# Performance work log

Hardware: AMD Instinct MI355X
Metric: run time of the kernel (lower is better)

The kernel has to match this reference:

```python
import jax, jax.numpy as jnp
import numpy as np

IN_FEATS = 256
HIDDEN = [256, 128]
N_SRC1, N_DST1, E1 = 262144, 32768, 524288
N_DST2, E2 = 4096, 65536


def _linear_params(key, out_f, in_f):
    kw, kb = jax.random.split(key)
    gain = float(np.sqrt(2.0))  # relu gain (xavier_uniform)
    bound = gain * float(np.sqrt(6.0 / (in_f + out_f)))
    W = jax.random.uniform(kw, (out_f, in_f), jnp.float32, -bound, bound)
    b = jax.random.uniform(kb, (out_f,), jnp.float32, -0.05, 0.05)
    return W, b


def setup_inputs() -> dict:
    key = jax.random.key(0)
    ks = jax.random.split(key, 16)
    x = jax.random.normal(ks[0], (N_SRC1, IN_FEATS), jnp.float32)
    src1 = jax.random.randint(ks[1], (E1,), 0, N_SRC1, jnp.int32)
    dst1 = jax.random.randint(ks[2], (E1,), 0, N_DST1, jnp.int32)
    w1 = jax.random.uniform(ks[3], (E1,), jnp.float32)
    src2 = jax.random.randint(ks[4], (E2,), 0, N_DST1, jnp.int32)
    dst2 = jax.random.randint(ks[5], (E2,), 0, N_DST2, jnp.int32)
    w2 = jax.random.uniform(ks[6], (E2,), jnp.float32)
    pool_w1, pool_b1 = _linear_params(ks[7], IN_FEATS, IN_FEATS)
    self_w1, self_b1 = _linear_params(ks[8], HIDDEN[0], IN_FEATS)
    neigh_w1, neigh_b1 = _linear_params(ks[9], HIDDEN[0], IN_FEATS)
    pool_w2, pool_b2 = _linear_params(ks[10], HIDDEN[0], HIDDEN[0])
    self_w2, self_b2 = _linear_params(ks[11], HIDDEN[1], HIDDEN[0])
    neigh_w2, neigh_b2 = _linear_params(ks[12], HIDDEN[1], HIDDEN[0])
    return dict(x=x, src1=src1, dst1=dst1, w1=w1, src2=src2, dst2=dst2, w2=w2,
                pool_w1=pool_w1, pool_b1=pool_b1, self_w1=self_w1, self_b1=self_b1,
                neigh_w1=neigh_w1, neigh_b1=neigh_b1,
                pool_w2=pool_w2, pool_b2=pool_b2, self_w2=self_w2, self_b2=self_b2,
                neigh_w2=neigh_w2, neigh_b2=neigh_b2,
                n_dst1=N_DST1, n_dst2=N_DST2)


def _sage_pool_layer(h, src, dst, w, n_dst, pool_w, pool_b, self_w, self_b, neigh_w, neigh_b):
    h_dst = h[:n_dst]                                   # [n_dst, f_in]
    pooled = jax.nn.relu(h @ pool_w.T + pool_b)         # [n_src, f_in]
    msg = pooled[src] * w[:, None]                      # [E, f_in] (u_mul_e)
    neigh = jax.ops.segment_max(msg, dst, num_segments=n_dst)
    neigh = jnp.where(jnp.isfinite(neigh), neigh, 0.0)  # DGL: 0 for isolated dst
    return h_dst @ self_w.T + self_b + neigh @ neigh_w.T + neigh_b


def reference(x, src1, dst1, w1, src2, dst2, w2,
              pool_w1, pool_b1, self_w1, self_b1, neigh_w1, neigh_b1,
              pool_w2, pool_b2, self_w2, self_b2, neigh_w2, neigh_b2,
              n_dst1, n_dst2):
    h = _sage_pool_layer(x, src1, dst1, w1, n_dst1,
                         pool_w1, pool_b1, self_w1, self_b1, neigh_w1, neigh_b1)
    h = jax.nn.relu(h)  # inter-layer activation (dropout=0 in eval)
    h = _sage_pool_layer(h, src2, dst2, w2, n_dst2,
                         pool_w2, pool_b2, self_w2, self_b2, neigh_w2, neigh_b2)
    return h
```

## Files before the change

kernel.cpp:

```cpp
#include <hip/hip_runtime.h>
#include <hip/hip_bf16.h>


typedef __bf16 bf16x8 __attribute__((ext_vector_type(8)));
typedef float  f32x4  __attribute__((ext_vector_type(4)));

constexpr int NS1 = 262144, ND1 = 32768, E1C = 524288, ND2 = 4096, E2C = 65536;
constexpr int FK  = 256;
constexpr int LDP = 40;

__device__ __forceinline__ void cvt_store(unsigned short* hi, unsigned short* lo,
                                          int off, float4 v)
{
    float f[4] = {v.x, v.y, v.z, v.w};
    ushort4 hs, ls;
    unsigned short* hp = &hs.x;
    unsigned short* lp = &ls.x;
#pragma unroll
    for (int e = 0; e < 4; ++e) {
        __bf16 h = (__bf16)f[e];
        __bf16 l = (__bf16)(f[e] - (float)h);
        hp[e] = __builtin_bit_cast(unsigned short, h);
        lp[e] = __builtin_bit_cast(unsigned short, l);
    }
    *(ushort4*)(hi + off) = hs;
    *(ushort4*)(lo + off) = ls;
}

__device__ __forceinline__ bf16x8 load_frag(const unsigned short* p)
{
    f32x4 t = *(const f32x4*)p;
    return __builtin_bit_cast(bf16x8, t);
}

template<int BM, int BN, bool RELU, bool DUAL>
__global__ __launch_bounds__(256, 2)
void mfma_gemm(const float* __restrict__ A, const float* __restrict__ W,
               const float* __restrict__ b1v,
               const float* __restrict__ A2, const float* __restrict__ W2,
               const float* __restrict__ b2v,
               float* __restrict__ C, int M, int N, int K)
{
    constexpr int RF  = BM / 32;
    constexpr int CF  = BN / 32;
    constexpr int AF4 = BM / 32;
    constexpr int BF4 = BN / 32;
    static_assert(RF >= 1 && CF >= 1 && BM % 32 == 0 && BN % 32 == 0, "tile");

    __shared__ unsigned short Ah[BM * LDP], Al[BM * LDP];
    __shared__ unsigned short Bh[BN * LDP], Bl[BN * LDP];

    const int tid  = threadIdx.x;
    const int wid  = tid >> 6, lane = tid & 63;
    const int wr   = wid >> 1, wc = wid & 1;
    const int lq   = lane >> 4, lr = lane & 15;
    const int m0   = blockIdx.x * BM;
    const int n0   = blockIdx.y * BN;

    f32x4 acc[RF][CF] = {};

    const int nkt = K / 32;
    const int tkt = DUAL ? 2 * nkt : nkt;

    float4 pv[AF4 + BF4];

    auto LOADP = [&](int kt) {
        const float* Ap = A;
        const float* Wp = W;
        int kb = kt * 32;
        if (DUAL && kt >= nkt) { Ap = A2; Wp = W2; kb = (kt - nkt) * 32; }
#pragma unroll
        for (int i = 0; i < AF4; ++i) {
            const int c = tid + i * 256;
            const int row = c >> 3, k0 = (c & 7) * 4;
            pv[i] = *(const float4*)(Ap + (size_t)(m0 + row) * K + kb + k0);
        }
#pragma unroll
        for (int i = 0; i < BF4; ++i) {
            const int c = tid + i * 256;
            const int row = c >> 3, k0 = (c & 7) * 4;
            pv[AF4 + i] = *(const float4*)(Wp + (size_t)(n0 + row) * K + kb + k0);
        }
    };

    LOADP(0);

    for (int kt = 0; kt < tkt; ++kt) {
#pragma unroll
        for (int i = 0; i < AF4; ++i) {
            const int c = tid + i * 256;
            const int row = c >> 3, k0 = (c & 7) * 4;
            cvt_store(Ah, Al, row * LDP + k0, pv[i]);
        }
#pragma unroll
        for (int i = 0; i < BF4; ++i) {
            const int c = tid + i * 256;
            const int row = c >> 3, k0 = (c & 7) * 4;
            cvt_store(Bh, Bl, row * LDP + k0, pv[AF4 + i]);
        }
        __syncthreads();

        if (kt + 1 < tkt) LOADP(kt + 1);

        bf16x8 ah[RF], al[RF];
#pragma unroll
        for (int i = 0; i < RF; ++i) {
            const int off = (wr * (BM / 2) + i * 16 + lr) * LDP + lq * 8;
            ah[i] = load_frag(Ah + off);
            al[i] = load_frag(Al + off);
        }
#pragma unroll
        for (int j = 0; j < CF; ++j) {
            const int off = (wc * (BN / 2) + j * 16 + lr) * LDP + lq * 8;
            const bf16x8 bh = load_frag(Bh + off);
            const bf16x8 bl = load_frag(Bl + off);
#pragma unroll
            for (int i = 0; i < RF; ++i) {
                acc[i][j] = __builtin_amdgcn_mfma_f32_16x16x32_bf16(ah[i], bh, acc[i][j], 0, 0, 0);
                acc[i][j] = __builtin_amdgcn_mfma_f32_16x16x32_bf16(ah[i], bl, acc[i][j], 0, 0, 0);
                acc[i][j] = __builtin_amdgcn_mfma_f32_16x16x32_bf16(al[i], bh, acc[i][j], 0, 0, 0);
            }
        }
        __syncthreads();
    }

#pragma unroll
    for (int j = 0; j < CF; ++j) {
        const int col = n0 + wc * (BN / 2) + j * 16 + lr;
        float bias = b1v[col];
        if constexpr (DUAL) bias += b2v[col];
#pragma unroll
        for (int i = 0; i < RF; ++i) {
            const int rbase = m0 + wr * (BM / 2) + i * 16 + lq * 4;
#pragma unroll
            for (int r = 0; r < 4; ++r) {
                float o = acc[i][j][r] + bias;
                if (RELU) o = fmaxf(o, 0.0f);
                C[(size_t)(rbase + r) * N + col] = o;
            }
        }
    }
}

__global__ __launch_bounds__(256)
void hist_kernel(const int* __restrict__ dst, int* __restrict__ cnt)
{
    const int e = blockIdx.x * 256 + threadIdx.x;
    atomicAdd(&cnt[dst[e]], 1);
}

template<int PT>
__global__ __launch_bounds__(1024)
void scan_kernel(int* __restrict__ a)
{
    __shared__ int s[1024];
    const int t = threadIdx.x;
    int v[PT];
    int sum = 0;
#pragma unroll
    for (int k = 0; k < PT; ++k) { v[k] = a[t * PT + k]; sum += v[k]; }
    s[t] = sum;
    __syncthreads();
    for (int off = 1; off < 1024; off <<= 1) {
        int x = (t >= off) ? s[t - off] : 0;
        __syncthreads();
        s[t] += x;
        __syncthreads();
    }
    int excl = (t == 0) ? 0 : s[t - 1];
#pragma unroll
    for (int k = 0; k < PT; ++k) { int x = v[k]; a[t * PT + k] = excl; excl += x; }
}

__global__ __launch_bounds__(256)
void scatter_kernel(const int* __restrict__ dst, int* __restrict__ cursor,
                    int* __restrict__ eids)
{
    const int e = blockIdx.x * 256 + threadIdx.x;
    const int p = atomicAdd(&cursor[dst[e]], 1);
    eids[p] = e;
}

__global__ __launch_bounds__(256)
void csr_agg_kernel(const float* __restrict__ pooled,
                    const int* __restrict__ srcA, const float* __restrict__ wA,
                    const int* __restrict__ eids, const int* __restrict__ cursor,
                    float* __restrict__ neigh, int ND)
{
    const int wid  = (blockIdx.x * 256 + threadIdx.x) >> 6;
    const int lane = threadIdx.x & 63;
    if (wid >= ND) return;

    const int start = wid ? cursor[wid - 1] : 0;
    const int end   = cursor[wid];

    float4 m = {0.0f, 0.0f, 0.0f, 0.0f};
    for (int e = start; e < end; ++e) {
        const int   eid = eids[e];
        const int   s   = srcA[eid];
        const float ww  = wA[eid];
        const float4 p  = *(const float4*)(pooled + (size_t)s * FK + lane * 4);
        m.x = fmaxf(m.x, p.x * ww);
        m.y = fmaxf(m.y, p.y * ww);
        m.z = fmaxf(m.z, p.z * ww);
        m.w = fmaxf(m.w, p.w * ww);
    }
    *(float4*)(neigh + (size_t)wid * FK + lane * 4) = m;
}

extern "C" void kernel_launch(void* const* d_in, const int* in_sizes, int n_in,
                              void* d_out, int out_size, void* d_ws, size_t ws_size,
                              hipStream_t stream)
{
    const float* x        = (const float*)d_in[0];
    const int*   src1     = (const int*)d_in[1];
    const int*   dst1     = (const int*)d_in[2];
    const float* w1       = (const float*)d_in[3];
    const int*   src2     = (const int*)d_in[4];
    const int*   dst2     = (const int*)d_in[5];
    const float* w2       = (const float*)d_in[6];
    const float* pool_w1  = (const float*)d_in[7];
    const float* pool_b1  = (const float*)d_in[8];
    const float* self_w1  = (const float*)d_in[9];
    const float* self_b1  = (const float*)d_in[10];
    const float* neigh_w1 = (const float*)d_in[11];
    const float* neigh_b1 = (const float*)d_in[12];
    const float* pool_w2  = (const float*)d_in[13];
    const float* pool_b2  = (const float*)d_in[14];
    const float* self_w2  = (const float*)d_in[15];
    const float* self_b2  = (const float*)d_in[16];
    const float* neigh_w2 = (const float*)d_in[17];
    const float* neigh_b2 = (const float*)d_in[18];

    char* ws = (char*)d_ws;
    float* pooled1 = (float*)ws;
    float* neigh1  = (float*)(ws + (size_t)NS1 * FK * 4);
    float* h2      = (float*)ws;
    float* pooled2 = (float*)(ws + (size_t)ND1 * FK * 4);
    float* neigh2  = (float*)(ws + (size_t)2 * ND1 * FK * 4);
    char*  csrbase = ws + (size_t)NS1 * FK * 4 + (size_t)ND1 * FK * 4;
    int*   cursor1 = (int*)csrbase;
    int*   eids2   = (int*)(csrbase + 131072);
    int*   cursor2 = (int*)(csrbase + 131072 + 262144);
    int*   eids1   = (int*)d_out;
    float* out     = (float*)d_out;

    hipMemsetAsync(cursor1, 0, ND1 * 4, stream);
    hipMemsetAsync(cursor2, 0, ND2 * 4, stream);
    hist_kernel<<<E1C / 256, 256, 0, stream>>>(dst1, cursor1);
    hist_kernel<<<E2C / 256, 256, 0, stream>>>(dst2, cursor2);
    scan_kernel<32><<<1, 1024, 0, stream>>>(cursor1);
    scan_kernel<4><<<1, 1024, 0, stream>>>(cursor2);
    scatter_kernel<<<E1C / 256, 256, 0, stream>>>(dst1, cursor1, eids1);
    scatter_kernel<<<E2C / 256, 256, 0, stream>>>(dst2, cursor2, eids2);

    mfma_gemm<128, 256, true, false>
        <<<dim3(NS1 / 128, 1), 256, 0, stream>>>(
            x, pool_w1, pool_b1, nullptr, nullptr, nullptr, pooled1, NS1, FK, FK);

    csr_agg_kernel<<<ND1 / 4, 256, 0, stream>>>(pooled1, src1, w1, eids1, cursor1,
                                                neigh1, ND1);

    mfma_gemm<128, 256, true, true>
        <<<dim3(ND1 / 128, 1), 256, 0, stream>>>(
            x, self_w1, self_b1, neigh1, neigh_w1, neigh_b1, h2, ND1, FK, FK);

    mfma_gemm<128, 256, true, false>
        <<<dim3(ND1 / 128, 1), 256, 0, stream>>>(
            h2, pool_w2, pool_b2, nullptr, nullptr, nullptr, pooled2, ND1, FK, FK);

    csr_agg_kernel<<<ND2 / 4, 256, 0, stream>>>(pooled2, src2, w2, eids2, cursor2,
                                                neigh2, ND2);

    mfma_gemm<64, 128, false, true>
        <<<dim3(ND2 / 64, 1), 256, 0, stream>>>(
            h2, self_w2, self_b2, neigh2, neigh_w2, neigh_b2, out, ND2, 128, FK);
}
```

Before: 769.3 us.

## Pre-split weights to bf16 hi/lo and stream them into LDS directly

Adds a small kernel that splits each weight matrix into bf16 high/low halves once per call. The GEMM then loads the B tiles straight into LDS with global_load_lds using an XOR swizzle, which removes the per-tile register round trip and the float-to-bf16 conversion for weights. It also raises wave priority around the MFMA block and unrolls the CSR max-aggregation loop by four to keep more gathers in flight. The cost is extra launches, workspace placed at fixed offsets, and added complexity in the swizzle indexing.

```diff
diff --git a/kernel.cpp b/kernel.cpp
--- a/kernel.cpp
+++ b/kernel.cpp
@@ -9,20 +9,20 @@
 constexpr int FK  = 256;
 constexpr int LDP = 40;
 
+__device__ __forceinline__ void split2(float f, unsigned short& h, unsigned short& l)
+{
+    __bf16 hb = (__bf16)f;
+    __bf16 lb = (__bf16)(f - (float)hb);
+    h = __builtin_bit_cast(unsigned short, hb);
+    l = __builtin_bit_cast(unsigned short, lb);
+}
+
 __device__ __forceinline__ void cvt_store(unsigned short* hi, unsigned short* lo,
                                           int off, float4 v)
 {
-    float f[4] = {v.x, v.y, v.z, v.w};
     ushort4 hs, ls;
-    unsigned short* hp = &hs.x;
-    unsigned short* lp = &ls.x;
-#pragma unroll
-    for (int e = 0; e < 4; ++e) {
-        __bf16 h = (__bf16)f[e];
-        __bf16 l = (__bf16)(f[e] - (float)h);
-        hp[e] = __builtin_bit_cast(unsigned short, h);
-        lp[e] = __builtin_bit_cast(unsigned short, l);
-    }
+    split2(v.x, hs.x, ls.x); split2(v.y, hs.y, ls.y);
+    split2(v.z, hs.z, ls.z); split2(v.w, hs.w, ls.w);
     *(ushort4*)(hi + off) = hs;
     *(ushort4*)(lo + off) = ls;
 }
@@ -33,22 +33,45 @@
     return __builtin_bit_cast(bf16x8, t);
 }
 
+__device__ __forceinline__ void gld_lds16(const void* g, void* l)
+{
+    __builtin_amdgcn_global_load_lds(
+        (const __attribute__((address_space(1))) unsigned int*)g,
+        (__attribute__((address_space(3))) unsigned int*)l, 16, 0, 0);
+}
+
+__global__ __launch_bounds__(256)
+void wsplit_kernel(const float* __restrict__ w, unsigned short* __restrict__ h,
+                   unsigned short* __restrict__ l, int n4)
+{
+    const int i = blockIdx.x * 256 + threadIdx.x;
+    if (i >= n4) return;
+    const float4 v = ((const float4*)w)[i];
+    ushort4 hs, ls;
+    split2(v.x, hs.x, ls.x); split2(v.y, hs.y, ls.y);
+    split2(v.z, hs.z, ls.z); split2(v.w, hs.w, ls.w);
+    ((ushort4*)h)[i] = hs;
+    ((ushort4*)l)[i] = ls;
+}
+
 template<int BM, int BN, bool RELU, bool DUAL>
 __global__ __launch_bounds__(256, 2)
-void mfma_gemm(const float* __restrict__ A, const float* __restrict__ W,
-               const float* __restrict__ b1v,
-               const float* __restrict__ A2, const float* __restrict__ W2,
-               const float* __restrict__ b2v,
-               float* __restrict__ C, int M, int N, int K)
-{
-    constexpr int RF  = BM / 32;
-    constexpr int CF  = BN / 32;
-    constexpr int AF4 = BM / 32;
-    constexpr int BF4 = BN / 32;
-    static_assert(RF >= 1 && CF >= 1 && BM % 32 == 0 && BN % 32 == 0, "tile");
-
-    __shared__ unsigned short Ah[BM * LDP], Al[BM * LDP];
-    __shared__ unsigned short Bh[BN * LDP], Bl[BN * LDP];
+void mfma_gemm2(const float* __restrict__ A,
+                const unsigned short* __restrict__ Wh, const unsigned short* __restrict__ Wl,
+                const float* __restrict__ b1v,
+                const float* __restrict__ A2,
+                const unsigned short* __restrict__ Wh2, const unsigned short* __restrict__ Wl2,
+                const float* __restrict__ b2v,
+                float* __restrict__ C, int M, int N, int K)
+{
+    constexpr int RF   = BM / 32;
+    constexpr int CF   = BN / 32;
+    constexpr int AF4  = BM / 32;
+    constexpr int BSEG = BN / 64;
+    static_assert(BM % 32 == 0 && BN % 64 == 0, "tile");
+
+    __shared__ alignas(16) unsigned short Ah[BM * LDP], Al[BM * LDP];
+    __shared__ alignas(16) unsigned short Bh[BN * 32], Bl[BN * 32];
 
     const int tid  = threadIdx.x;
     const int wid  = tid >> 6, lane = tid & 63;
@@ -56,51 +79,53 @@
     const int lq   = lane >> 4, lr = lane & 15;
     const int m0   = blockIdx.x * BM;
     const int n0   = blockIdx.y * BN;
+    const int rloc = lane >> 2;
+    const int cld  = lane & 3;
 
     f32x4 acc[RF][CF] = {};
-
     const int nkt = K / 32;
     const int tkt = DUAL ? 2 * nkt : nkt;
 
-    float4 pv[AF4 + BF4];
-
-    auto LOADP = [&](int kt) {
+    float4 pv[AF4];
+    auto LOADA = [&](int kt) {
         const float* Ap = A;
-        const float* Wp = W;
         int kb = kt * 32;
-        if (DUAL && kt >= nkt) { Ap = A2; Wp = W2; kb = (kt - nkt) * 32; }
+        if (DUAL && kt >= nkt) { Ap = A2; kb = (kt - nkt) * 32; }
 #pragma unroll
         for (int i = 0; i < AF4; ++i) {
             const int c = tid + i * 256;
             const int row = c >> 3, k0 = (c & 7) * 4;
             pv[i] = *(const float4*)(Ap + (size_t)(m0 + row) * K + kb + k0);
         }
-#pragma unroll
-        for (int i = 0; i < BF4; ++i) {
-            const int c = tid + i * 256;
-            const int row = c >> 3, k0 = (c & 7) * 4;
-            pv[AF4 + i] = *(const float4*)(Wp + (size_t)(n0 + row) * K + kb + k0);
-        }
     };
 
-    LOADP(0);
+    LOADA(0);
 
     for (int kt = 0; kt < tkt; ++kt) {
+        {
+            const unsigned short* Ph = Wh;
+            const unsigned short* Pl = Wl;
+            int kb = kt * 32;
+            if (DUAL && kt >= nkt) { Ph = Wh2; Pl = Wl2; kb = (kt - nkt) * 32; }
+#pragma unroll
+            for (int c = 0; c < BSEG; ++c) {
+                const int seg = wid * BSEG + c;
+                const int row = seg * 16 + rloc;
+                const int cg  = cld ^ ((row >> 1) & 3);
+                const size_t gofs = (size_t)(n0 + row) * K + kb + cg * 8;
+                gld_lds16(Ph + gofs, Bh + seg * 512);
+                gld_lds16(Pl + gofs, Bl + seg * 512);
+            }
+        }
 #pragma unroll
         for (int i = 0; i < AF4; ++i) {
             const int c = tid + i * 256;
             const int row = c >> 3, k0 = (c & 7) * 4;
             cvt_store(Ah, Al, row * LDP + k0, pv[i]);
         }
-#pragma unroll
-        for (int i = 0; i < BF4; ++i) {
-            const int c = tid + i * 256;
-            const int row = c >> 3, k0 = (c & 7) * 4;
-            cvt_store(Bh, Bl, row * LDP + k0, pv[AF4 + i]);
-        }
         __syncthreads();
 
-        if (kt + 1 < tkt) LOADP(kt + 1);
+        if (kt + 1 < tkt) LOADA(kt + 1);
 
         bf16x8 ah[RF], al[RF];
 #pragma unroll
@@ -109,9 +134,11 @@
             ah[i] = load_frag(Ah + off);
             al[i] = load_frag(Al + off);
         }
+        __builtin_amdgcn_s_setprio(1);
 #pragma unroll
         for (int j = 0; j < CF; ++j) {
-            const int off = (wc * (BN / 2) + j * 16 + lr) * LDP + lq * 8;
+            const int R   = wc * (BN / 2) + j * 16 + lr;
+            const int off = R * 32 + (lq ^ ((R >> 1) & 3)) * 8;
             const bf16x8 bh = load_frag(Bh + off);
             const bf16x8 bl = load_frag(Bl + off);
 #pragma unroll
@@ -121,6 +148,7 @@
                 acc[i][j] = __builtin_amdgcn_mfma_f32_16x16x32_bf16(al[i], bh, acc[i][j], 0, 0, 0);
             }
         }
+        __builtin_amdgcn_s_setprio(0);
         __syncthreads();
     }
 
@@ -195,7 +223,21 @@
     const int end   = cursor[wid];
 
     float4 m = {0.0f, 0.0f, 0.0f, 0.0f};
-    for (int e = start; e < end; ++e) {
+    int e = start;
+    for (; e + 3 < end; e += 4) {
+        const int eid0 = eids[e], eid1 = eids[e + 1], eid2 = eids[e + 2], eid3 = eids[e + 3];
+        const int s0 = srcA[eid0], s1 = srcA[eid1], s2 = srcA[eid2], s3 = srcA[eid3];
+        const float w0 = wA[eid0], w1 = wA[eid1], w2 = wA[eid2], w3 = wA[eid3];
+        const float4 p0 = *(const float4*)(pooled + (size_t)s0 * FK + lane * 4);
+        const float4 p1 = *(const float4*)(pooled + (size_t)s1 * FK + lane * 4);
+        const float4 p2 = *(const float4*)(pooled + (size_t)s2 * FK + lane * 4);
+        const float4 p3 = *(const float4*)(pooled + (size_t)s3 * FK + lane * 4);
+        m.x = fmaxf(fmaxf(m.x, p0.x * w0), fmaxf(p1.x * w1, fmaxf(p2.x * w2, p3.x * w3)));
+        m.y = fmaxf(fmaxf(m.y, p0.y * w0), fmaxf(p1.y * w1, fmaxf(p2.y * w2, p3.y * w3)));
+        m.z = fmaxf(fmaxf(m.z, p0.z * w0), fmaxf(p1.z * w1, fmaxf(p2.z * w2, p3.z * w3)));
+        m.w = fmaxf(fmaxf(m.w, p0.w * w0), fmaxf(p1.w * w1, fmaxf(p2.w * w2, p3.w * w3)));
+    }
+    for (; e < end; ++e) {
         const int   eid = eids[e];
         const int   s   = srcA[eid];
         const float ww  = wA[eid];
@@ -245,6 +287,15 @@
     int*   eids1   = (int*)d_out;
     float* out     = (float*)d_out;
 
+    unsigned short* pw1h = (unsigned short*)(ws + (size_t)NS1 * FK * 4);
+    unsigned short* pw1l = pw1h + 65536;
+    unsigned short* WB   = (unsigned short*)(ws + (size_t)96 * 1024 * 1024);
+    unsigned short* sw1h = WB;           unsigned short* sw1l = WB + 65536;
+    unsigned short* nw1h = WB + 131072;  unsigned short* nw1l = WB + 196608;
+    unsigned short* pw2h = WB + 262144;  unsigned short* pw2l = WB + 327680;
+    unsigned short* sw2h = WB + 393216;  unsigned short* sw2l = WB + 425984;
+    unsigned short* nw2h = WB + 458752;  unsigned short* nw2l = WB + 491520;
+
     hipMemsetAsync(cursor1, 0, ND1 * 4, stream);
     hipMemsetAsync(cursor2, 0, ND2 * 4, stream);
     hist_kernel<<<E1C / 256, 256, 0, stream>>>(dst1, cursor1);
@@ -254,25 +305,37 @@
     scatter_kernel<<<E1C / 256, 256, 0, stream>>>(dst1, cursor1, eids1);
     scatter_kernel<<<E2C / 256, 256, 0, stream>>>(dst2, cursor2, eids2);
 
-    mfma_gemm<128, 256, true, false>
+    wsplit_kernel<<<64, 256, 0, stream>>>(pool_w1, pw1h, pw1l, 65536 / 4);
+
+    mfma_gemm2<128, 256, true, false>
         <<<dim3(NS1 / 128, 1), 256, 0, stream>>>(
-            x, pool_w1, pool_b1, nullptr, nullptr, nullptr, pooled1, NS1, FK, FK);
+            x, pw1h, pw1l, pool_b1, nullptr, nullptr, nullptr, nullptr,
+            pooled1, NS1, FK, FK);
 
     csr_agg_kernel<<<ND1 / 4, 256, 0, stream>>>(pooled1, src1, w1, eids1, cursor1,
                                                 neigh1, ND1);
 
-    mfma_gemm<128, 256, true, true>
+    wsplit_kernel<<<64, 256, 0, stream>>>(self_w1,  sw1h, sw1l, 65536 / 4);
+    wsplit_kernel<<<64, 256, 0, stream>>>(neigh_w1, nw1h, nw1l, 65536 / 4);
+    wsplit_kernel<<<64, 256, 0, stream>>>(pool_w2,  pw2h, pw2l, 65536 / 4);
+    wsplit_kernel<<<32, 256, 0, stream>>>(self_w2,  sw2h, sw2l, 32768 / 4);
+    wsplit_kernel<<<32, 256, 0, stream>>>(neigh_w2, nw2h, nw2l, 32768 / 4);
+
+    mfma_gemm2<128, 256, true, true>
         <<<dim3(ND1 / 128, 1), 256, 0, stream>>>(
-            x, self_w1, self_b1, neigh1, neigh_w1, neigh_b1, h2, ND1, FK, FK);
-
-    mfma_gemm<128, 256, true, false>
+            x, sw1h, sw1l, self_b1, neigh1, nw1h, nw1l, neigh_b1,
+            h2, ND1, FK, FK);
+
+    mfma_gemm2<128, 256, true, false>
         <<<dim3(ND1 / 128, 1), 256, 0, stream>>>(
-            h2, pool_w2, pool_b2, nullptr, nullptr, nullptr, pooled2, ND1, FK, FK);
+            h2, pw2h, pw2l, pool_b2, nullptr, nullptr, nullptr, nullptr,
+            pooled2, ND1, FK, FK);
 
     csr_agg_kernel<<<ND2 / 4, 256, 0, stream>>>(pooled2, src2, w2, eids2, cursor2,
                                                 neigh2, ND2);
 
-    mfma_gemm<64, 128, false, true>
+    mfma_gemm2<64, 128, false, true>
         <<<dim3(ND2 / 64, 1), 256, 0, stream>>>(
-            h2, self_w2, self_b2, neigh2, neigh_w2, neigh_b2, out, ND2, 128, FK);
-}
+            h2, sw2h, sw2l, self_b2, neigh2, nw2h, nw2l, neigh_b2,
+            out, ND2, 128, FK);
+}
```

New measurement: 721.3 us. 6.2% less time.
